# Kernel optimization log

Measured on AMD Instinct MI355X. Metric: run time of the kernel, lower is better.

Reference implementation:

```python
import jax, jax.numpy as jnp
import numpy as np

VERTS = [5023, 1256, 314, 79, 20]
SPIRAL_LEN = 9
T_FRAMES = 32
LATENT = 64


def _spiral_conv(x, idx, W, b):
    # x: [B, N, C]; idx: [N, L]; gather spiral neighborhoods then linear
    B = x.shape[0]
    g = x[:, idx.reshape(-1), :].reshape(B, idx.shape[0], -1)  # [B, N, L*C]
    return g @ W.T + b


def _pool(x, rows, cols, vals, n_out):
    # sparse matmul: out[b, rows] += x[b, cols] * vals  (index_select + scatter_add)
    gathered = x[:, cols, :] * vals[None, :, None]
    return jnp.zeros((x.shape[0], n_out, x.shape[2]), x.dtype).at[:, rows, :].add(gathered)


def _lstm_dir(x, Wih, Whh, bih, bhh, reverse):
    # x: [T, B, D]; PyTorch gate order i, f, g, o
    Bz, H = x.shape[1], Whh.shape[1]
    bias = bih + bhh
    def step(carry, xt):
        h, c = carry
        g = xt @ Wih.T + h @ Whh.T + bias
        i, f, gg, o = jnp.split(g, 4, axis=-1)
        c = jax.nn.sigmoid(f) * c + jax.nn.sigmoid(i) * jnp.tanh(gg)
        h = jax.nn.sigmoid(o) * jnp.tanh(c)
        return (h, c), h
    init = (jnp.zeros((Bz, H), x.dtype), jnp.zeros((Bz, H), x.dtype))
    _, hs = jax.lax.scan(step, init, x, reverse=reverse)
    return hs


def _forward(audio_hidden, vertices, actor,
             sp_idx0, sp_idx1, sp_idx2, sp_idx3,
             d0_rows, d0_cols, d0_vals, d1_rows, d1_cols, d1_vals,
             d2_rows, d2_cols, d2_vals, d3_rows, d3_cols, d3_vals,
             u0_rows, u0_cols, u0_vals, u1_rows, u1_cols, u1_vals,
             u2_rows, u2_cols, u2_vals, u3_rows, u3_cols, u3_vals,
             enc_W0, enc_b0, enc_W1, enc_b1, enc_W2, enc_b2, enc_W3, enc_b3,
             enc_lin_W, enc_lin_b, dec_lin_W, dec_lin_b,
             dec_W0, dec_b0, dec_W1, dec_b1, dec_W2, dec_b2, dec_W3, dec_b3,
             dec_W4, dec_b4, aud_W, aud_b,
             l0_Wih, l0_Whh, l0_bih, l0_bhh, l12_Wih, l12_Whh, l12_bih, l12_bhh):
    ah = audio_hidden
    if ah.shape[1] % 2 != 0:
        ah = ah[:, :ah.shape[1] - 1]
    tv = vertices.shape[1]
    if ah.shape[1] > 2 * tv:
        ah = ah[:, :2 * tv]
    elif ah.shape[1] < 2 * tv:
        tv = ah.shape[1] // 2
    hs = ah.reshape(1, ah.shape[1] // 2, ah.shape[2] * 2)[:, :tv]  # [1, T, 1536]
    audio_emb = hs @ aud_W.T + aud_b                                # [1, T, LATENT]
    # --- mesh encoder on actor template: (spiral conv -> ELU -> down pool) x4 -> Linear ---
    sp = (sp_idx0, sp_idx1, sp_idx2, sp_idx3)
    down = ((d0_rows, d0_cols, d0_vals), (d1_rows, d1_cols, d1_vals),
            (d2_rows, d2_cols, d2_vals), (d3_rows, d3_cols, d3_vals))
    encp = ((enc_W0, enc_b0), (enc_W1, enc_b1), (enc_W2, enc_b2), (enc_W3, enc_b3))
    x = actor
    for i in range(4):
        x = jax.nn.elu(_spiral_conv(x, sp[i], *encp[i]))
        x = _pool(x, *down[i], VERTS[i + 1])
    z = x.reshape(x.shape[0], -1) @ enc_lin_W.T + enc_lin_b        # [1, LATENT]
    actor_emb = jnp.broadcast_to(z[:, None, :], audio_emb.shape)
    # --- 3-layer bidirectional LSTM ---
    h = jnp.concatenate([audio_emb, actor_emb], axis=-1).transpose(1, 0, 2)  # [T, 1, 2*LATENT]
    for layer in range(3):
        if layer == 0:
            Wih, Whh, bih, bhh = l0_Wih, l0_Whh, l0_bih, l0_bhh
        else:
            Wih, Whh, bih, bhh = l12_Wih[layer - 1], l12_Whh[layer - 1], l12_bih[layer - 1], l12_bhh[layer - 1]
        f = _lstm_dir(h, Wih[0], Whh[0], bih[0], bhh[0], False)
        r = _lstm_dir(h, Wih[1], Whh[1], bih[1], bhh[1], True)
        h = jnp.concatenate([f, r], axis=-1)
    latent = h.transpose(1, 0, 2)[0]                               # [T, LATENT]
    # --- mesh decoder, batched over all frames (replaces the python per-frame loop) ---
    up = ((u0_rows, u0_cols, u0_vals), (u1_rows, u1_cols, u1_vals),
          (u2_rows, u2_cols, u2_vals), (u3_rows, u3_cols, u3_vals))
    decp = ((dec_W0, dec_b0), (dec_W1, dec_b1), (dec_W2, dec_b2), (dec_W3, dec_b3))
    y = latent @ dec_lin_W.T + dec_lin_b                           # [T, 20*256]
    y = y.reshape(y.shape[0], VERTS[4], -1)                        # [T, 20, 256]
    for i in range(4):
        j = 3 - i
        y = _pool(y, *up[j], VERTS[j])
        y = jax.nn.elu(_spiral_conv(y, sp[j], *decp[i]))
    y = _spiral_conv(y, sp[0], dec_W4, dec_b4)                     # [T, 5023, 3]
    return y + actor                                               # broadcast residual, == vstacked preds


def setup_inputs() -> dict:
    key = jax.random.key(0)
    ks = iter(jax.random.split(key, 96))
    def nrm(shape, s=0.05):
        return jax.random.normal(next(ks), shape, jnp.float32) * s
    def rint(shape, hi):
        return jax.random.randint(next(ks), shape, 0, hi)
    inp = {}
    inp['audio_hidden'] = nrm((1, 2 * T_FRAMES, 768), 1.0)
    inp['vertices'] = nrm((1, T_FRAMES, VERTS[0], 3), 1.0)
    inp['actor'] = nrm((1, VERTS[0], 3), 1.0)
    for i in range(4):
        inp['sp_idx%d' % i] = rint((VERTS[i], SPIRAL_LEN), VERTS[i])
    for i in range(4):
        nnz = 3 * VERTS[i + 1]
        inp['d%d_rows' % i] = rint((nnz,), VERTS[i + 1])
        inp['d%d_cols' % i] = rint((nnz,), VERTS[i])
        inp['d%d_vals' % i] = jax.random.uniform(next(ks), (nnz,), jnp.float32)
    for i in range(4):
        nnz = 3 * VERTS[i]
        inp['u%d_rows' % i] = rint((nnz,), VERTS[i])
        inp['u%d_cols' % i] = rint((nnz,), VERTS[i + 1])
        inp['u%d_vals' % i] = jax.random.uniform(next(ks), (nnz,), jnp.float32)
    OC = [32, 64, 128, 256]
    ic = 3
    for i in range(4):
        inp['enc_W%d' % i] = nrm((OC[i], ic * SPIRAL_LEN))
        inp['enc_b%d' % i] = nrm((OC[i],))
        ic = OC[i]
    inp['enc_lin_W'] = nrm((LATENT, VERTS[4] * OC[3]))
    inp['enc_lin_b'] = nrm((LATENT,))
    inp['dec_lin_W'] = nrm((VERTS[4] * OC[3], LATENT))
    inp['dec_lin_b'] = nrm((VERTS[4] * OC[3],))
    dic = [256, 256, 128, 64]
    doc = [256, 128, 64, 32]
    for i in range(4):
        inp['dec_W%d' % i] = nrm((doc[i], dic[i] * SPIRAL_LEN))
        inp['dec_b%d' % i] = nrm((doc[i],))
    inp['dec_W4'] = nrm((3, OC[0] * SPIRAL_LEN))
    inp['dec_b4'] = nrm((3,))
    inp['aud_W'] = nrm((LATENT, 1536))
    inp['aud_b'] = nrm((LATENT,))
    H = LATENT // 2
    inp['l0_Wih'] = nrm((2, 4 * H, 2 * LATENT))
    inp['l0_Whh'] = nrm((2, 4 * H, H))
    inp['l0_bih'] = nrm((2, 4 * H))
    inp['l0_bhh'] = nrm((2, 4 * H))
    inp['l12_Wih'] = nrm((2, 2, 4 * H, 2 * H))
    inp['l12_Whh'] = nrm((2, 2, 4 * H, H))
    inp['l12_bih'] = nrm((2, 2, 4 * H))
    inp['l12_bhh'] = nrm((2, 2, 4 * H))
    return inp


def reference(audio_hidden, vertices, actor,
              sp_idx0, sp_idx1, sp_idx2, sp_idx3,
              d0_rows, d0_cols, d0_vals, d1_rows, d1_cols, d1_vals,
              d2_rows, d2_cols, d2_vals, d3_rows, d3_cols, d3_vals,
              u0_rows, u0_cols, u0_vals, u1_rows, u1_cols, u1_vals,
              u2_rows, u2_cols, u2_vals, u3_rows, u3_cols, u3_vals,
              enc_W0, enc_b0, enc_W1, enc_b1, enc_W2, enc_b2, enc_W3, enc_b3,
              enc_lin_W, enc_lin_b, dec_lin_W, dec_lin_b,
              dec_W0, dec_b0, dec_W1, dec_b1, dec_W2, dec_b2, dec_W3, dec_b3,
              dec_W4, dec_b4, aud_W, aud_b,
              l0_Wih, l0_Whh, l0_bih, l0_bhh, l12_Wih, l12_Whh, l12_bih, l12_bhh):
    return _forward(audio_hidden, vertices, actor,
                    sp_idx0, sp_idx1, sp_idx2, sp_idx3,
                    d0_rows, d0_cols, d0_vals, d1_rows, d1_cols, d1_vals,
                    d2_rows, d2_cols, d2_vals, d3_rows, d3_cols, d3_vals,
                    u0_rows, u0_cols, u0_vals, u1_rows, u1_cols, u1_vals,
                    u2_rows, u2_cols, u2_vals, u3_rows, u3_cols, u3_vals,
                    enc_W0, enc_b0, enc_W1, enc_b1, enc_W2, enc_b2, enc_W3, enc_b3,
                    enc_lin_W, enc_lin_b, dec_lin_W, dec_lin_b,
                    dec_W0, dec_b0, dec_W1, dec_b1, dec_W2, dec_b2, dec_W3, dec_b3,
                    dec_W4, dec_b4, aud_W, aud_b,
                    l0_Wih, l0_Whh, l0_bih, l0_bhh, l12_Wih, l12_Whh, l12_bih, l12_bhh)
```

## Files before the change

kernel.cpp:

```cpp
#include <hip/hip_runtime.h>
#include <cstdint>
#include <cstddef>


typedef unsigned short u16;
typedef __attribute__((ext_vector_type(8))) short short8;
typedef __attribute__((ext_vector_type(4))) float float4v;
#define CDIV(a,b) (((a)+(b)-1)/(b))
#define POOL_CAP 64

__device__ __forceinline__ float bf(u16 u){ return __uint_as_float(((unsigned)u)<<16); }
__device__ __forceinline__ u16 fb(float x){
  unsigned u = __float_as_uint(x);
  unsigned r = u + 0x7fffu + ((u>>16)&1u);
  return (u16)(r>>16);
}
__device__ __forceinline__ float lo16(unsigned u){ return __uint_as_float(u<<16); }
__device__ __forceinline__ float hi16(unsigned u){ return __uint_as_float(u & 0xffff0000u); }

struct WCast { const float* src[7]; int cum[8]; };
struct Lists {
  const int* rows[8];
  int nnz[8];
  int curoff[8];
  int lstoff[8];
};

__global__ void __launch_bounds__(256) setup_k(
    Lists L, int totN, int NF, int* __restrict__ curBase, int* __restrict__ lstBase,
    WCast C, int totW, int NC, u16* __restrict__ Wbf,
    const float* __restrict__ audio, const float* __restrict__ audW,
    const float* __restrict__ audB, float* __restrict__ h0,
    const float* __restrict__ actor, const int* __restrict__ sp0,
    const float* __restrict__ encW0, const float* __restrict__ encB0,
    u16* __restrict__ outA){
  int blk = blockIdx.x;
  int tid = threadIdx.x;
  if (blk < NF){
    int i = blk*256 + tid;
    if (i < totN){
      int off = i, k = 0;
      while (off >= L.nnz[k]){ off -= L.nnz[k]; k++; }
      int r = L.rows[k][off];
      int p = atomicAdd(curBase + L.curoff[k] + r, 1);
      if (p < POOL_CAP) lstBase[L.lstoff[k] + r*POOL_CAP + p] = off;
    }
    return;
  }
  blk -= NF;
  if (blk < NC){
    int i = blk*256 + tid;
    if (i < totW){
      int k = 0;
      while (i >= C.cum[k+1]) k++;
      Wbf[i] = fb(C.src[k][i - C.cum[k]]);
    }
    return;
  }
  blk -= NC;
  if (blk < 32){
    int t = blk;
    int f = tid >> 2, sl = tid & 3;
    const float4* x4 = (const float4*)(audio + t*1536);
    const float4* w4 = (const float4*)(audW + f*1536);
    float acc = 0.f;
    for (int k=sl; k<384; k+=4){
      float4 xv = x4[k], wv = w4[k];
      acc += xv.x*wv.x + xv.y*wv.y + xv.z*wv.z + xv.w*wv.w;
    }
    acc += __shfl_down(acc, 2, 64);
    acc += __shfl_down(acc, 1, 64);
    if (sl == 0) h0[t*128 + f] = acc + audB[f];
    return;
  }
  blk -= 32;
  int i = blk*256 + tid;
  if (i >= 5023*32) return;
  int o = i % 32; int v = i / 32;
  const float* wrow = encW0 + (size_t)o*27;
  const int* vix = sp0 + v*9;
  float acc = encB0[o];
  for (int s=0;s<9;s++){
    const float* xr = actor + (size_t)vix[s]*3;
    acc += xr[0]*wrow[s*3] + xr[1]*wrow[s*3+1] + xr[2]*wrow[s*3+2];
  }
  if (acc < 0.f) acc = expm1f(acc);
  outA[i] = fb(acc);
}

template<int IC, int BN, int BM>
__global__ void __launch_bounds__(256) conv_mfma(
    const u16* __restrict__ x, const int* __restrict__ idx,
    const u16* __restrict__ Wb, const float* __restrict__ bias,
    u16* __restrict__ out, int V, int OC, int M){
  constexpr int K = 9*IC;
  constexpr int KC = K/32;
  constexpr int NT = BN/16;
  constexpr int MT = BM/64;
  constexpr int LOG2 = (IC==32?5: IC==64?6: IC==128?7:8);
  constexpr int AST = 40;
  __shared__ u16 Asm[2][BM*AST];
  __shared__ u16 Bsm[2][BN*AST];
  __shared__ int rowB[BM], rowV[BM];
  __shared__ int sidx[BM*9];
  int t = threadIdx.x;
  int m0 = blockIdx.x*BM;
  int o0 = blockIdx.y*BN;
  if (t < BM){
    int mg = m0 + t;
    if (mg < M){ int b = mg / V; rowB[t] = b; rowV[t] = mg - b*V; }
    else rowB[t] = -1;
  }
  __syncthreads();
  for (int i=t; i<BM*9; i+=256){
    int r = i/9, s = i - r*9;
    sidx[i] = (rowB[r] >= 0) ? idx[rowV[r]*9 + s] : 0;
  }
  int lane = t & 63, wave = t >> 6;
  int quad = lane >> 4, col = lane & 15;
  float4v acc[MT][NT];
  #pragma unroll
  for (int mi=0;mi<MT;mi++)
    #pragma unroll
    for (int nt=0;nt<NT;nt++) acc[mi][nt] = (float4v)0.f;

  uint4 aval[MT]; uint4 bval;
  auto fetch = [&](int kc){
    int s  = (kc*32) >> LOG2;
    int c0 = (kc*32) & (IC-1);
    #pragma unroll
    for (int rpt=0; rpt<MT; ++rpt){
      int seg = t + 256*rpt;
      int arow = seg >> 2, aq = seg & 3;
      int b = rowB[arow];
      uint4 v = {0u,0u,0u,0u};
      if (b >= 0){
        int ix = sidx[arow*9 + s];
        v = *(const uint4*)(x + ((size_t)b*V + ix)*IC + c0 + aq*8);
      }
      aval[rpt] = v;
    }
    if (t < BN*4){
      int br = t >> 2, bq = t & 3;
      bval = *(const uint4*)(Wb + (size_t)(o0+br)*K + kc*32 + bq*8);
    }
  };

  __syncthreads();
  fetch(0);

  for (int kc = 0; kc < KC; ++kc){
    int buf = kc & 1;
    #pragma unroll
    for (int rpt=0; rpt<MT; ++rpt){
      int seg = t + 256*rpt;
      int arow = seg >> 2, aq = seg & 3;
      *(uint4*)&Asm[buf][arow*AST + aq*8] = aval[rpt];
    }
    if (t < BN*4){
      int br = t >> 2, bq = t & 3;
      *(uint4*)&Bsm[buf][br*AST + bq*8] = bval;
    }
    __syncthreads();
    if (kc+1 < KC) fetch(kc+1);
    short8 a[MT];
    #pragma unroll
    for (int mi=0;mi<MT;mi++)
      a[mi] = *(const short8*)&Asm[buf][(wave*MT*16 + mi*16 + col)*AST + quad*8];
    #pragma unroll
    for (int nt=0; nt<NT; ++nt){
      short8 bfr = *(const short8*)&Bsm[buf][(nt*16 + col)*AST + quad*8];
      #pragma unroll
      for (int mi=0;mi<MT;mi++)
        acc[mi][nt] = __builtin_amdgcn_mfma_f32_16x16x32_bf16(a[mi], bfr, acc[mi][nt], 0, 0, 0);
    }
  }
  #pragma unroll
  for (int mi=0;mi<MT;mi++){
    #pragma unroll
    for (int nt=0; nt<NT; ++nt){
      int o = o0 + nt*16 + col;
      float bv = bias[o];
      #pragma unroll
      for (int r=0;r<4;r++){
        int mg = m0 + wave*MT*16 + mi*16 + quad*4 + r;
        if (mg < M){
          float val = acc[mi][nt][r] + bv;
          if (val < 0.f) val = expm1f(val);
          out[(size_t)mg*OC + o] = fb(val);
        }
      }
    }
  }
}

__global__ void pool_g8_k(const u16* __restrict__ x, const int* __restrict__ cols,
                          const float* __restrict__ vals, const int* __restrict__ cur,
                          const int* __restrict__ lst, u16* __restrict__ out,
                          int B, int Vin, int Vout, int C){
  int C8 = C >> 3;
  int total = B*Vout*C8;
  int i = blockIdx.x*blockDim.x + threadIdx.x;
  if (i >= total) return;
  int c8 = i % C8; int tt = i / C8; int r = tt % Vout; int b = tt / Vout;
  int deg = cur[r]; if (deg > POOL_CAP) deg = POOL_CAP;
  const int* le = lst + r*POOL_CAP;
  float a0=0.f,a1=0.f,a2=0.f,a3=0.f,a4=0.f,a5=0.f,a6=0.f,a7=0.f;
  for (int k=0;k<deg;k++){
    int e = le[k];
    float v = vals[e];
    uint4 xv = *(const uint4*)(x + ((size_t)b*Vin + (size_t)cols[e])*C + c8*8);
    a0 += v*lo16(xv.x); a1 += v*hi16(xv.x);
    a2 += v*lo16(xv.y); a3 += v*hi16(xv.y);
    a4 += v*lo16(xv.z); a5 += v*hi16(xv.z);
    a6 += v*lo16(xv.w); a7 += v*hi16(xv.w);
  }
  uint4 o;
  o.x = ((unsigned)fb(a0)) | (((unsigned)fb(a1))<<16);
  o.y = ((unsigned)fb(a2)) | (((unsigned)fb(a3))<<16);
  o.z = ((unsigned)fb(a4)) | (((unsigned)fb(a5))<<16);
  o.w = ((unsigned)fb(a6)) | (((unsigned)fb(a7))<<16);
  *(uint4*)(out + ((size_t)b*Vout + (size_t)r)*C + c8*8) = o;
}

__global__ void __launch_bounds__(256) enc_lin_k(
    const u16* __restrict__ x, const float* __restrict__ W,
    const float* __restrict__ b, float* __restrict__ h0){
  int f = blockIdx.x;
  int t = threadIdx.x;
  const ushort4* x4 = (const ushort4*)x;
  const float4* w4 = (const float4*)(W + (size_t)f*5120);
  float acc = 0.f;
  for (int k=t; k<1280; k+=256){
    ushort4 xv = x4[k]; float4 wv = w4[k];
    acc += bf(xv.x)*wv.x + bf(xv.y)*wv.y + bf(xv.z)*wv.z + bf(xv.w)*wv.w;
  }
  #pragma unroll
  for (int off=32; off; off>>=1) acc += __shfl_down(acc, off, 64);
  __shared__ float red[4];
  if ((t & 63) == 0) red[t>>6] = acc;
  __syncthreads();
  if (t < 32){
    float zf = b[f] + red[0] + red[1] + red[2] + red[3];
    h0[t*128 + 64 + f] = zf;
  }
}

__device__ __forceinline__ float sigm(float x){ return 1.f/(1.f+__expf(-x)); }
__device__ __forceinline__ float tanhfast(float x){ return 1.f - 2.f/(__expf(2.f*x)+1.f); }

__global__ void __launch_bounds__(256) lstm3_k(
    const float* __restrict__ h0,
    const float* __restrict__ l0_Wih, const float* __restrict__ l0_Whh,
    const float* __restrict__ l0_bih, const float* __restrict__ l0_bhh,
    const float* __restrict__ l12_Wih, const float* __restrict__ l12_Whh,
    const float* __restrict__ l12_bih, const float* __restrict__ l12_bhh,
    float* __restrict__ latent){
  __shared__ __align__(16) u16 xb[32*136];
  __shared__ __align__(16) float xp[2*32*128];
  __shared__ __align__(16) u16 obuf[32*64];
  __shared__ __align__(16) float hsh32[2][32];
  __shared__ float bias_l[256];
  int t = threadIdx.x;
  int lane = t & 63, wave = t >> 6;
  int quad = lane >> 4, col = lane & 15;

  for (int i=t;i<32*128;i+=256){ int tt=i>>7, k=i&127; xb[tt*136+k]=fb(h0[i]); }

  for (int layer=0; layer<3; layer++){
    int IN = (layer==0)?128:64;
    const float *Wih,*Whh,*bih,*bhh;
    if (layer==0){ Wih=l0_Wih; Whh=l0_Whh; bih=l0_bih; bhh=l0_bhh; }
    else {
      int mb=(layer-1)*2;
      Wih=l12_Wih + (size_t)mb*128*64; Whh=l12_Whh + (size_t)mb*128*32;
      bih=l12_bih + mb*128; bhh=l12_bhh + mb*128;
    }
    bias_l[t] = bih[(t>>7)*128 + (t&127)] + bhh[(t>>7)*128 + (t&127)];
    __syncthreads();

    {
      int dirA = wave >> 1, o0 = (wave & 1)*64;
      const float* WA = Wih + (size_t)dirA*128*IN;
      float4v acc[2][4];
      #pragma unroll
      for (int mi=0;mi<2;mi++)
        #pragma unroll
        for (int nt=0;nt<4;nt++) acc[mi][nt] = (float4v)0.f;
      for (int kc=0; kc<IN/32; ++kc){
        short8 bfrag[4];
        #pragma unroll
        for (int nt=0;nt<4;nt++){
          const float* src = WA + (size_t)(o0+nt*16+col)*IN + kc*32 + quad*8;
          float4 w0 = *(const float4*)src;
          float4 w1 = *(const float4*)(src+4);
          alignas(16) u16 tmp[8] = {fb(w0.x),fb(w0.y),fb(w0.z),fb(w0.w),
                                    fb(w1.x),fb(w1.y),fb(w1.z),fb(w1.w)};
          bfrag[nt] = *(const short8*)tmp;
        }
        short8 afrag[2];
        #pragma unroll
        for (int mi=0;mi<2;mi++)
          afrag[mi] = *(const short8*)&xb[(mi*16+col)*136 + kc*32 + quad*8];
        #pragma unroll
        for (int nt=0;nt<4;nt++)
          #pragma unroll
          for (int mi=0;mi<2;mi++)
            acc[mi][nt] = __builtin_amdgcn_mfma_f32_16x16x32_bf16(afrag[mi], bfrag[nt], acc[mi][nt], 0, 0, 0);
      }
      #pragma unroll
      for (int mi=0;mi<2;mi++)
        #pragma unroll
        for (int nt=0;nt<4;nt++){
          int j = o0 + nt*16 + col;
          float bv = bias_l[dirA*128 + j];
          #pragma unroll
          for (int r=0;r<4;r++){
            int tt = mi*16 + quad*4 + r;
            xp[dirA*4096 + tt*128 + j] = acc[mi][nt][r] + bv;
          }
        }
    }
    __syncthreads();

    if (wave < 2){
      int dir = wave; bool rev = (dir == 1);
      int unit = lane & 31, gh = lane >> 5;
      int jA = gh*32 + unit;
      int jB = (gh+2)*32 + unit;
      const float* WD = Whh + (size_t)dir*128*32;
      float wA[32], wB[32];
      #pragma unroll
      for (int k=0;k<32;k++){ wA[k]=WD[(size_t)jA*32+k]; wB[k]=WD[(size_t)jB*32+k]; }
      float* hsd = &hsh32[dir][0];
      if (gh==0) hsd[unit] = 0.f;
      float creg = 0.f;
      const float* xpd = xp + dir*4096;
      float gAc = xpd[(rev?31:0)*128 + jA];
      float gBc = xpd[(rev?31:0)*128 + jB];
      #pragma unroll 1
      for (int s=0;s<32;s++){
        int tx = rev ? (31-s) : s;
        int sn = (s+1 < 32) ? s+1 : 31;
        int txn = rev ? (31-sn) : sn;
        float gA2 = xpd[txn*128 + jA];
        float gB2 = xpd[txn*128 + jB];
        const float4* h4 = (const float4*)hsd;
        float a0=0.f,a1=0.f,a2=0.f,a3=0.f,b0=0.f,b1=0.f,b2=0.f,b3=0.f;
        #pragma unroll
        for (int k=0;k<8;k++){
          float4 hv = h4[k];
          a0=fmaf(hv.x,wA[4*k+0],a0); b0=fmaf(hv.x,wB[4*k+0],b0);
          a1=fmaf(hv.y,wA[4*k+1],a1); b1=fmaf(hv.y,wB[4*k+1],b1);
          a2=fmaf(hv.z,wA[4*k+2],a2); b2=fmaf(hv.z,wB[4*k+2],b2);
          a3=fmaf(hv.w,wA[4*k+3],a3); b3=fmaf(hv.w,wB[4*k+3],b3);
        }
        float gA = gAc + ((a0+a1)+(a2+a3));
        float gB = gBc + ((b0+b1)+(b2+b3));
        float actA = sigm(gA);
        float tB = sigm(gh ? gB : 2.f*gB);
        float actB = gh ? tB : (2.f*tB - 1.f);
        float pA = __shfl_xor(actA, 32, 64);
        float pB = __shfl_xor(actB, 32, 64);
        float gi = gh ? pA : actA;
        float gf = gh ? actA : pA;
        float gg = gh ? pB : actB;
        float go = gh ? actB : pB;
        float cn = fmaf(gf, creg, gi*gg);
        float hn = go * tanhfast(cn);
        creg = cn;
        if (gh==0){
          hsd[unit] = hn;
          obuf[tx*64 + dir*32 + unit] = fb(hn);
        }
        gAc = gA2; gBc = gB2;
      }
    }
    __syncthreads();
    if (layer < 2){
      for (int i=t;i<32*64;i+=256){ int tt=i>>6, k=i&63; xb[tt*136+k]=obuf[i]; }
      __syncthreads();
    }
  }
  for (int i=t;i<32*64;i+=256) latent[i] = bf(obuf[i]);
}

__global__ void dec_lin_k(const float* __restrict__ latent, const float* __restrict__ W,
                          const float* __restrict__ b, u16* __restrict__ y){
  int i = blockIdx.x*blockDim.x + threadIdx.x;
  if (i >= 32*5120) return;
  int r = i % 5120, t = i / 5120;
  const float4* x4 = (const float4*)(latent + t*64);
  const float4* w4 = (const float4*)(W + (size_t)r*64);
  float acc = b[r];
  #pragma unroll
  for (int k=0;k<16;k++){
    float4 xv=x4[k]; float4 wv=w4[k];
    acc += xv.x*wv.x+xv.y*wv.y+xv.z*wv.z+xv.w*wv.w;
  }
  y[i] = fb(acc);
}

__global__ void final_k(const u16* __restrict__ x, const int* __restrict__ idx,
                        const float* __restrict__ W, const float* __restrict__ bias,
                        const float* __restrict__ actor, float* __restrict__ out){
  __shared__ float Wsm[3*288];
  __shared__ float bsm[3];
  int t = threadIdx.x;
  for (int i=t;i<864;i+=256) Wsm[i]=W[i];
  if (t<3) bsm[t]=bias[t];
  __syncthreads();
  int g = blockIdx.x*256 + t;
  if (g >= 32*5023) return;
  int v = g % 5023, b = g / 5023;
  const u16* xb = x + (size_t)b*5023*32;
  const int* vix = idx + v*9;
  float a0=bsm[0], a1=bsm[1], a2=bsm[2];
  for (int s=0;s<9;s++){
    const ushort4* xr = (const ushort4*)(xb + (size_t)vix[s]*32);
    #pragma unroll
    for (int k=0;k<8;k++){
      ushort4 xv = xr[k];
      float x0=bf(xv.x), x1=bf(xv.y), x2=bf(xv.z), x3=bf(xv.w);
      int kk = s*32 + k*4;
      a0 += x0*Wsm[kk] + x1*Wsm[kk+1] + x2*Wsm[kk+2] + x3*Wsm[kk+3];
      a1 += x0*Wsm[288+kk] + x1*Wsm[288+kk+1] + x2*Wsm[288+kk+2] + x3*Wsm[288+kk+3];
      a2 += x0*Wsm[576+kk] + x1*Wsm[576+kk+1] + x2*Wsm[576+kk+2] + x3*Wsm[576+kk+3];
    }
  }
  out[(size_t)g*3+0] = a0 + actor[v*3+0];
  out[(size_t)g*3+1] = a1 + actor[v*3+1];
  out[(size_t)g*3+2] = a2 + actor[v*3+2];
}

extern "C" void kernel_launch(void* const* d_in, const int* in_sizes, int n_in,
                              void* d_out, int out_size, void* d_ws, size_t ws_size,
                              hipStream_t stream){
  (void)in_sizes; (void)n_in; (void)out_size; (void)ws_size;

  const float* audio = (const float*)d_in[0];
  const float* actor = (const float*)d_in[2];
  const int* sp[4]   = {(const int*)d_in[3],(const int*)d_in[4],(const int*)d_in[5],(const int*)d_in[6]};
  const int* drows[4]; const int* dcols[4]; const float* dvals[4];
  for (int i=0;i<4;i++){ drows[i]=(const int*)d_in[7+3*i]; dcols[i]=(const int*)d_in[8+3*i]; dvals[i]=(const float*)d_in[9+3*i]; }
  const int* urows[4]; const int* ucols[4]; const float* uvals[4];
  for (int i=0;i<4;i++){ urows[i]=(const int*)d_in[19+3*i]; ucols[i]=(const int*)d_in[20+3*i]; uvals[i]=(const float*)d_in[21+3*i]; }
  const float* encW[4]={(const float*)d_in[31],(const float*)d_in[33],(const float*)d_in[35],(const float*)d_in[37]};
  const float* encB[4]={(const float*)d_in[32],(const float*)d_in[34],(const float*)d_in[36],(const float*)d_in[38]};
  const float* enc_lin_W=(const float*)d_in[39]; const float* enc_lin_b=(const float*)d_in[40];
  const float* dec_lin_W=(const float*)d_in[41]; const float* dec_lin_b=(const float*)d_in[42];
  const float* decW[5]={(const float*)d_in[43],(const float*)d_in[45],(const float*)d_in[47],(const float*)d_in[49],(const float*)d_in[51]};
  const float* decB[5]={(const float*)d_in[44],(const float*)d_in[46],(const float*)d_in[48],(const float*)d_in[50],(const float*)d_in[52]};
  const float* audW=(const float*)d_in[53]; const float* audB=(const float*)d_in[54];
  const float* l0_Wih=(const float*)d_in[55]; const float* l0_Whh=(const float*)d_in[56];
  const float* l0_bih=(const float*)d_in[57]; const float* l0_bhh=(const float*)d_in[58];
  const float* l12_Wih=(const float*)d_in[59]; const float* l12_Whh=(const float*)d_in[60];
  const float* l12_bih=(const float*)d_in[61]; const float* l12_bhh=(const float*)d_in[62];
  float* out = (float*)d_out;

  char* base = (char*)d_ws;
  u16* A  = (u16*)base;
  u16* Bb = (u16*)(base + 10287104);
  int* curBase = (int*)(base + 30891520);
  int* lstBase = (int*)(base + 30924928);
  u16* Wbf = (u16*)(base + 33060224);
  float* sm = (float*)(base + 35788160);
  float* h0     = sm;
  float* latent = sm + 4096;

  const int wsz[7] = {64*288, 128*576, 256*1152, 256*2304, 128*2304, 64*1152, 32*576};
  WCast WC; int wcum = 0;
  const float* wsrc[7] = {encW[1],encW[2],encW[3],decW[0],decW[1],decW[2],decW[3]};
  int wo[7];
  for (int k=0;k<7;k++){ WC.src[k]=wsrc[k]; WC.cum[k]=wcum; wo[k]=wcum; wcum+=wsz[k]; }
  WC.cum[7]=wcum;

  const int pVout[8] = {1256,314,79,20,5023,1256,314,79};
  const int pNnz[8]  = {3768,942,237,60,15069,3768,942,237};
  Lists L; int curoff=0, lstoff=0, totnnz=0;
  const int* prow[8] = {drows[0],drows[1],drows[2],drows[3],urows[0],urows[1],urows[2],urows[3]};
  int curo[8], lsto[8];
  for (int k=0;k<8;k++){
    L.rows[k]=prow[k]; L.nnz[k]=pNnz[k];
    L.curoff[k]=curoff; L.lstoff[k]=lstoff;
    curo[k]=curoff; lsto[k]=lstoff;
    curoff += pVout[k]; lstoff += pVout[k]*POOL_CAP; totnnz += pNnz[k];
  }
  hipMemsetAsync(curBase, 0, (size_t)curoff*4, stream);

  int NF = CDIV(totnnz,256), NC = CDIV(wcum,256), NC3 = CDIV(5023*32,256);
  setup_k<<<NF+NC+32+NC3,256,0,stream>>>(L, totnnz, NF, curBase, lstBase,
                                         WC, wcum, NC, Wbf,
                                         audio, audW, audB, h0,
                                         actor, sp[0], encW[0], encB[0], A);

  pool_g8_k<<<CDIV(1256*4,256),256,0,stream>>>(A, dcols[0], dvals[0], curBase+curo[0], lstBase+lsto[0], Bb, 1, 5023, 1256, 32);
  conv_mfma<32,64,64><<<dim3(CDIV(1256,64),1),256,0,stream>>>(Bb, sp[1], Wbf+wo[0], encB[1], A, 1256, 64, 1256);
  pool_g8_k<<<CDIV(314*8,256),256,0,stream>>>(A, dcols[1], dvals[1], curBase+curo[1], lstBase+lsto[1], Bb, 1, 1256, 314, 64);
  conv_mfma<64,64,64><<<dim3(CDIV(314,64),2),256,0,stream>>>(Bb, sp[2], Wbf+wo[1], encB[2], A, 314, 128, 314);
  pool_g8_k<<<CDIV(79*16,256),256,0,stream>>>(A, dcols[2], dvals[2], curBase+curo[2], lstBase+lsto[2], Bb, 1, 314, 79, 128);
  conv_mfma<128,64,64><<<dim3(CDIV(79,64),4),256,0,stream>>>(Bb, sp[3], Wbf+wo[2], encB[3], A, 79, 256, 79);
  pool_g8_k<<<CDIV(20*32,256),256,0,stream>>>(A, dcols[3], dvals[3], curBase+curo[3], lstBase+lsto[3], Bb, 1, 79, 20, 256);

  enc_lin_k<<<64,256,0,stream>>>(Bb, enc_lin_W, enc_lin_b, h0);

  lstm3_k<<<1,256,0,stream>>>(h0, l0_Wih, l0_Whh, l0_bih, l0_bhh,
                              l12_Wih, l12_Whh, l12_bih, l12_bhh, latent);

  dec_lin_k<<<CDIV(32*5120,256),256,0,stream>>>(latent, dec_lin_W, dec_lin_b, A);

  pool_g8_k<<<CDIV(32*79*32,256),256,0,stream>>>(A, ucols[3], uvals[3], curBase+curo[7], lstBase+lsto[7], Bb, 32, 20, 79, 256);
  conv_mfma<256,64,64><<<dim3(CDIV(2528,64),4),256,0,stream>>>(Bb, sp[3], Wbf+wo[3], decB[0], A, 79, 256, 2528);

  pool_g8_k<<<CDIV(32*314*32,256),256,0,stream>>>(A, ucols[2], uvals[2], curBase+curo[6], lstBase+lsto[6], Bb, 32, 79, 314, 256);
  conv_mfma<256,64,64><<<dim3(CDIV(10048,64),2),256,0,stream>>>(Bb, sp[2], Wbf+wo[4], decB[1], A, 314, 128, 10048);

  pool_g8_k<<<CDIV(32*1256*16,256),256,0,stream>>>(A, ucols[1], uvals[1], curBase+curo[5], lstBase+lsto[5], Bb, 32, 314, 1256, 128);
  conv_mfma<128,64,128><<<dim3(CDIV(40192,128),1),256,0,stream>>>(Bb, sp[1], Wbf+wo[5], decB[2], A, 1256, 64, 40192);

  pool_g8_k<<<CDIV(32*5023*8,256),256,0,stream>>>(A, ucols[0], uvals[0], curBase+curo[4], lstBase+lsto[4], Bb, 32, 1256, 5023, 64);
  conv_mfma<64,32,128><<<dim3(CDIV(160736,128),1),256,0,stream>>>(Bb, sp[0], Wbf+wo[6], decB[3], A, 5023, 32, 160736);

  final_k<<<CDIV(32*5023,256),256,0,stream>>>(A, sp[0], decW[4], decB[4], actor, out);
}
```

Baseline: 569.2 us.

## Fuse encoder and decoder stages into persistent megakernels with grid barriers

Replaces the chain of separate pool, conv, linear and final launches with two persistent kernels, one for the encoder (64 blocks) and one for the decoder (256 blocks). Each stage loops over its tiles with a grid-stride loop, and stages are separated by atomic-counter grid barriers whose counters are reset in the setup kernel. The aim is to remove per-launch overhead and tail gaps between many small kernels. In exchange the decoder's large conv stages now run on only 256 blocks with a fixed static shared-memory footprint, which may cut parallelism and occupancy. The spin barriers also assume every block is co-resident on the GPU.

```diff
diff --git a/kernel.cpp b/kernel.cpp
--- a/kernel.cpp
+++ b/kernel.cpp
@@ -17,6 +17,18 @@
 }
 __device__ __forceinline__ float lo16(unsigned u){ return __uint_as_float(u<<16); }
 __device__ __forceinline__ float hi16(unsigned u){ return __uint_as_float(u & 0xffff0000u); }
+
+__device__ __forceinline__ void gsync(int* cnt, int nblk){
+  __syncthreads();
+  if (threadIdx.x == 0){
+    __threadfence();
+    atomicAdd(cnt, 1);
+    while (atomicAdd(cnt, 0) < nblk)
+      __builtin_amdgcn_s_sleep(8);
+    __threadfence();
+  }
+  __syncthreads();
+}
 
 struct WCast { const float* src[7]; int cum[8]; };
 struct Lists {
@@ -33,9 +45,10 @@
     const float* __restrict__ audB, float* __restrict__ h0,
     const float* __restrict__ actor, const int* __restrict__ sp0,
     const float* __restrict__ encW0, const float* __restrict__ encB0,
-    u16* __restrict__ outA){
+    u16* __restrict__ outA, int* __restrict__ bar){
   int blk = blockIdx.x;
   int tid = threadIdx.x;
+  if (blk == 0 && tid < 32) bar[tid] = 0;
   if (blk < NF){
     int i = blk*256 + tid;
     if (i < totN){
@@ -88,8 +101,37 @@
   outA[i] = fb(acc);
 }
 
+struct PoolP { const int* cols; const float* vals; const int* cur; const int* lst;
+               int B, Vin, Vout, C; };
+
+__device__ void pool_dev(const u16* __restrict__ x, PoolP p, u16* __restrict__ out){
+  int C8 = p.C >> 3;
+  int total = p.B*p.Vout*C8;
+  for (int i = blockIdx.x*256 + threadIdx.x; i < total; i += gridDim.x*256){
+    int c8 = i % C8; int tt = i / C8; int r = tt % p.Vout; int b = tt / p.Vout;
+    int deg = p.cur[r]; if (deg > POOL_CAP) deg = POOL_CAP;
+    const int* le = p.lst + r*POOL_CAP;
+    float a0=0.f,a1=0.f,a2=0.f,a3=0.f,a4=0.f,a5=0.f,a6=0.f,a7=0.f;
+    for (int k=0;k<deg;k++){
+      int e = le[k];
+      float v = p.vals[e];
+      uint4 xv = *(const uint4*)(x + ((size_t)b*p.Vin + (size_t)p.cols[e])*p.C + c8*8);
+      a0 += v*lo16(xv.x); a1 += v*hi16(xv.x);
+      a2 += v*lo16(xv.y); a3 += v*hi16(xv.y);
+      a4 += v*lo16(xv.z); a5 += v*hi16(xv.z);
+      a6 += v*lo16(xv.w); a7 += v*hi16(xv.w);
+    }
+    uint4 o;
+    o.x = ((unsigned)fb(a0)) | (((unsigned)fb(a1))<<16);
+    o.y = ((unsigned)fb(a2)) | (((unsigned)fb(a3))<<16);
+    o.z = ((unsigned)fb(a4)) | (((unsigned)fb(a5))<<16);
+    o.w = ((unsigned)fb(a6)) | (((unsigned)fb(a7))<<16);
+    *(uint4*)(out + ((size_t)b*p.Vout + (size_t)r)*p.C + c8*8) = o;
+  }
+}
+
 template<int IC, int BN, int BM>
-__global__ void __launch_bounds__(256) conv_mfma(
+__device__ void conv_dev(char* smem,
     const u16* __restrict__ x, const int* __restrict__ idx,
     const u16* __restrict__ Wb, const float* __restrict__ bias,
     u16* __restrict__ out, int V, int OC, int M){
@@ -99,151 +141,243 @@
   constexpr int MT = BM/64;
   constexpr int LOG2 = (IC==32?5: IC==64?6: IC==128?7:8);
   constexpr int AST = 40;
-  __shared__ u16 Asm[2][BM*AST];
-  __shared__ u16 Bsm[2][BN*AST];
-  __shared__ int rowB[BM], rowV[BM];
-  __shared__ int sidx[BM*9];
+  u16* Asm0 = (u16*)smem;
+  u16* Bsm0 = Asm0 + 2*BM*AST;
+  int* rowB = (int*)(Bsm0 + 2*BN*AST);
+  int* rowV = rowB + BM;
+  int* sidx = rowV + BM;
   int t = threadIdx.x;
-  int m0 = blockIdx.x*BM;
-  int o0 = blockIdx.y*BN;
-  if (t < BM){
-    int mg = m0 + t;
-    if (mg < M){ int b = mg / V; rowB[t] = b; rowV[t] = mg - b*V; }
-    else rowB[t] = -1;
-  }
-  __syncthreads();
-  for (int i=t; i<BM*9; i+=256){
-    int r = i/9, s = i - r*9;
-    sidx[i] = (rowB[r] >= 0) ? idx[rowV[r]*9 + s] : 0;
-  }
   int lane = t & 63, wave = t >> 6;
   int quad = lane >> 4, col = lane & 15;
-  float4v acc[MT][NT];
-  #pragma unroll
-  for (int mi=0;mi<MT;mi++)
-    #pragma unroll
-    for (int nt=0;nt<NT;nt++) acc[mi][nt] = (float4v)0.f;
-
-  uint4 aval[MT]; uint4 bval;
-  auto fetch = [&](int kc){
-    int s  = (kc*32) >> LOG2;
-    int c0 = (kc*32) & (IC-1);
-    #pragma unroll
-    for (int rpt=0; rpt<MT; ++rpt){
-      int seg = t + 256*rpt;
-      int arow = seg >> 2, aq = seg & 3;
-      int b = rowB[arow];
-      uint4 v = {0u,0u,0u,0u};
-      if (b >= 0){
-        int ix = sidx[arow*9 + s];
-        v = *(const uint4*)(x + ((size_t)b*V + ix)*IC + c0 + aq*8);
-      }
-      aval[rpt] = v;
-    }
-    if (t < BN*4){
-      int br = t >> 2, bq = t & 3;
-      bval = *(const uint4*)(Wb + (size_t)(o0+br)*K + kc*32 + bq*8);
-    }
-  };
-
-  __syncthreads();
-  fetch(0);
-
-  for (int kc = 0; kc < KC; ++kc){
-    int buf = kc & 1;
-    #pragma unroll
-    for (int rpt=0; rpt<MT; ++rpt){
-      int seg = t + 256*rpt;
-      int arow = seg >> 2, aq = seg & 3;
-      *(uint4*)&Asm[buf][arow*AST + aq*8] = aval[rpt];
-    }
-    if (t < BN*4){
-      int br = t >> 2, bq = t & 3;
-      *(uint4*)&Bsm[buf][br*AST + bq*8] = bval;
+  int ntx = (M + BM - 1)/BM, nty = OC/BN;
+  int ntiles = ntx*nty;
+
+  for (int tile = blockIdx.x; tile < ntiles; tile += gridDim.x){
+    int m0 = (tile % ntx)*BM;
+    int o0 = (tile / ntx)*BN;
+    if (t < BM){
+      int mg = m0 + t;
+      if (mg < M){ int b = mg / V; rowB[t] = b; rowV[t] = mg - b*V; }
+      else rowB[t] = -1;
     }
     __syncthreads();
-    if (kc+1 < KC) fetch(kc+1);
-    short8 a[MT];
+    for (int i=t; i<BM*9; i+=256){
+      int r = i/9, s = i - r*9;
+      sidx[i] = (rowB[r] >= 0) ? idx[rowV[r]*9 + s] : 0;
+    }
+    float4v acc[MT][NT];
     #pragma unroll
     for (int mi=0;mi<MT;mi++)
-      a[mi] = *(const short8*)&Asm[buf][(wave*MT*16 + mi*16 + col)*AST + quad*8];
+      #pragma unroll
+      for (int nt=0;nt<NT;nt++) acc[mi][nt] = (float4v)0.f;
+
+    uint4 aval[MT]; uint4 bval;
+    auto fetch = [&](int kc){
+      int s  = (kc*32) >> LOG2;
+      int c0 = (kc*32) & (IC-1);
+      #pragma unroll
+      for (int rpt=0; rpt<MT; ++rpt){
+        int seg = t + 256*rpt;
+        int arow = seg >> 2, aq = seg & 3;
+        int b = rowB[arow];
+        uint4 v = {0u,0u,0u,0u};
+        if (b >= 0){
+          int ix = sidx[arow*9 + s];
+          v = *(const uint4*)(x + ((size_t)b*V + ix)*IC + c0 + aq*8);
+        }
+        aval[rpt] = v;
+      }
+      if (t < BN*4){
+        int br = t >> 2, bq = t & 3;
+        bval = *(const uint4*)(Wb + (size_t)(o0+br)*K + kc*32 + bq*8);
+      }
+    };
+
+    __syncthreads();
+    fetch(0);
+
+    for (int kc = 0; kc < KC; ++kc){
+      int buf = kc & 1;
+      #pragma unroll
+      for (int rpt=0; rpt<MT; ++rpt){
+        int seg = t + 256*rpt;
+        int arow = seg >> 2, aq = seg & 3;
+        *(uint4*)&Asm0[buf*BM*AST + arow*AST + aq*8] = aval[rpt];
+      }
+      if (t < BN*4){
+        int br = t >> 2, bq = t & 3;
+        *(uint4*)&Bsm0[buf*BN*AST + br*AST + bq*8] = bval;
+      }
+      __syncthreads();
+      if (kc+1 < KC) fetch(kc+1);
+      short8 a[MT];
+      #pragma unroll
+      for (int mi=0;mi<MT;mi++)
+        a[mi] = *(const short8*)&Asm0[buf*BM*AST + (wave*MT*16 + mi*16 + col)*AST + quad*8];
+      #pragma unroll
+      for (int nt=0; nt<NT; ++nt){
+        short8 bfr = *(const short8*)&Bsm0[buf*BN*AST + (nt*16 + col)*AST + quad*8];
+        #pragma unroll
+        for (int mi=0;mi<MT;mi++)
+          acc[mi][nt] = __builtin_amdgcn_mfma_f32_16x16x32_bf16(a[mi], bfr, acc[mi][nt], 0, 0, 0);
+      }
+    }
     #pragma unroll
-    for (int nt=0; nt<NT; ++nt){
-      short8 bfr = *(const short8*)&Bsm[buf][(nt*16 + col)*AST + quad*8];
-      #pragma unroll
-      for (int mi=0;mi<MT;mi++)
-        acc[mi][nt] = __builtin_amdgcn_mfma_f32_16x16x32_bf16(a[mi], bfr, acc[mi][nt], 0, 0, 0);
-    }
-  }
-  #pragma unroll
-  for (int mi=0;mi<MT;mi++){
+    for (int mi=0;mi<MT;mi++){
+      #pragma unroll
+      for (int nt=0; nt<NT; ++nt){
+        int o = o0 + nt*16 + col;
+        float bv = bias[o];
+        #pragma unroll
+        for (int r=0;r<4;r++){
+          int mg = m0 + wave*MT*16 + mi*16 + quad*4 + r;
+          if (mg < M){
+            float val = acc[mi][nt][r] + bv;
+            if (val < 0.f) val = expm1f(val);
+            out[(size_t)mg*OC + o] = fb(val);
+          }
+        }
+      }
+    }
+  }
+}
+
+__device__ void enc_lin_dev(char* smem, const u16* __restrict__ x,
+                            const float* __restrict__ W, const float* __restrict__ b,
+                            float* __restrict__ h0){
+  float* red = (float*)smem;
+  int t = threadIdx.x;
+  for (int f = blockIdx.x; f < 64; f += gridDim.x){
+    const ushort4* x4 = (const ushort4*)x;
+    const float4* w4 = (const float4*)(W + (size_t)f*5120);
+    float acc = 0.f;
+    for (int k=t; k<1280; k+=256){
+      ushort4 xv = x4[k]; float4 wv = w4[k];
+      acc += bf(xv.x)*wv.x + bf(xv.y)*wv.y + bf(xv.z)*wv.z + bf(xv.w)*wv.w;
+    }
     #pragma unroll
-    for (int nt=0; nt<NT; ++nt){
-      int o = o0 + nt*16 + col;
-      float bv = bias[o];
-      #pragma unroll
-      for (int r=0;r<4;r++){
-        int mg = m0 + wave*MT*16 + mi*16 + quad*4 + r;
-        if (mg < M){
-          float val = acc[mi][nt][r] + bv;
-          if (val < 0.f) val = expm1f(val);
-          out[(size_t)mg*OC + o] = fb(val);
-        }
-      }
-    }
-  }
-}
-
-__global__ void pool_g8_k(const u16* __restrict__ x, const int* __restrict__ cols,
-                          const float* __restrict__ vals, const int* __restrict__ cur,
-                          const int* __restrict__ lst, u16* __restrict__ out,
-                          int B, int Vin, int Vout, int C){
-  int C8 = C >> 3;
-  int total = B*Vout*C8;
-  int i = blockIdx.x*blockDim.x + threadIdx.x;
-  if (i >= total) return;
-  int c8 = i % C8; int tt = i / C8; int r = tt % Vout; int b = tt / Vout;
-  int deg = cur[r]; if (deg > POOL_CAP) deg = POOL_CAP;
-  const int* le = lst + r*POOL_CAP;
-  float a0=0.f,a1=0.f,a2=0.f,a3=0.f,a4=0.f,a5=0.f,a6=0.f,a7=0.f;
-  for (int k=0;k<deg;k++){
-    int e = le[k];
-    float v = vals[e];
-    uint4 xv = *(const uint4*)(x + ((size_t)b*Vin + (size_t)cols[e])*C + c8*8);
-    a0 += v*lo16(xv.x); a1 += v*hi16(xv.x);
-    a2 += v*lo16(xv.y); a3 += v*hi16(xv.y);
-    a4 += v*lo16(xv.z); a5 += v*hi16(xv.z);
-    a6 += v*lo16(xv.w); a7 += v*hi16(xv.w);
-  }
-  uint4 o;
-  o.x = ((unsigned)fb(a0)) | (((unsigned)fb(a1))<<16);
-  o.y = ((unsigned)fb(a2)) | (((unsigned)fb(a3))<<16);
-  o.z = ((unsigned)fb(a4)) | (((unsigned)fb(a5))<<16);
-  o.w = ((unsigned)fb(a6)) | (((unsigned)fb(a7))<<16);
-  *(uint4*)(out + ((size_t)b*Vout + (size_t)r)*C + c8*8) = o;
-}
-
-__global__ void __launch_bounds__(256) enc_lin_k(
-    const u16* __restrict__ x, const float* __restrict__ W,
-    const float* __restrict__ b, float* __restrict__ h0){
-  int f = blockIdx.x;
+    for (int off=32; off; off>>=1) acc += __shfl_down(acc, off, 64);
+    if ((t & 63) == 0) red[t>>6] = acc;
+    __syncthreads();
+    if (t < 32){
+      float zf = b[f] + red[0] + red[1] + red[2] + red[3];
+      h0[t*128 + 64 + f] = zf;
+    }
+    __syncthreads();
+  }
+}
+
+__device__ void dec_lin_dev(const float* __restrict__ latent, const float* __restrict__ W,
+                            const float* __restrict__ b, u16* __restrict__ y){
+  for (int i = blockIdx.x*256 + threadIdx.x; i < 32*5120; i += gridDim.x*256){
+    int r = i % 5120, tt = i / 5120;
+    const float4* x4 = (const float4*)(latent + tt*64);
+    const float4* w4 = (const float4*)(W + (size_t)r*64);
+    float acc = b[r];
+    #pragma unroll
+    for (int k=0;k<16;k++){
+      float4 xv=x4[k]; float4 wv=w4[k];
+      acc += xv.x*wv.x+xv.y*wv.y+xv.z*wv.z+xv.w*wv.w;
+    }
+    y[i] = fb(acc);
+  }
+}
+
+__device__ void final_dev(char* smem, const u16* __restrict__ x, const int* __restrict__ idx,
+                          const float* __restrict__ W, const float* __restrict__ bias,
+                          const float* __restrict__ actor, float* __restrict__ out){
+  float* Wsm = (float*)smem;
+  float* bsm = Wsm + 864;
   int t = threadIdx.x;
-  const ushort4* x4 = (const ushort4*)x;
-  const float4* w4 = (const float4*)(W + (size_t)f*5120);
-  float acc = 0.f;
-  for (int k=t; k<1280; k+=256){
-    ushort4 xv = x4[k]; float4 wv = w4[k];
-    acc += bf(xv.x)*wv.x + bf(xv.y)*wv.y + bf(xv.z)*wv.z + bf(xv.w)*wv.w;
-  }
-  #pragma unroll
-  for (int off=32; off; off>>=1) acc += __shfl_down(acc, off, 64);
-  __shared__ float red[4];
-  if ((t & 63) == 0) red[t>>6] = acc;
+  for (int i=t;i<864;i+=256) Wsm[i]=W[i];
+  if (t<3) bsm[t]=bias[t];
   __syncthreads();
-  if (t < 32){
-    float zf = b[f] + red[0] + red[1] + red[2] + red[3];
-    h0[t*128 + 64 + f] = zf;
-  }
+  for (int g = blockIdx.x*256 + t; g < 32*5023; g += gridDim.x*256){
+    int v = g % 5023, b = g / 5023;
+    const u16* xb = x + (size_t)b*5023*32;
+    const int* vix = idx + v*9;
+    float a0=bsm[0], a1=bsm[1], a2=bsm[2];
+    for (int s=0;s<9;s++){
+      const ushort4* xr = (const ushort4*)(xb + (size_t)vix[s]*32);
+      #pragma unroll
+      for (int k=0;k<8;k++){
+        ushort4 xv = xr[k];
+        float x0=bf(xv.x), x1=bf(xv.y), x2=bf(xv.z), x3=bf(xv.w);
+        int kk = s*32 + k*4;
+        a0 += x0*Wsm[kk] + x1*Wsm[kk+1] + x2*Wsm[kk+2] + x3*Wsm[kk+3];
+        a1 += x0*Wsm[288+kk] + x1*Wsm[288+kk+1] + x2*Wsm[288+kk+2] + x3*Wsm[288+kk+3];
+        a2 += x0*Wsm[576+kk] + x1*Wsm[576+kk+1] + x2*Wsm[576+kk+2] + x3*Wsm[576+kk+3];
+      }
+    }
+    out[(size_t)g*3+0] = a0 + actor[v*3+0];
+    out[(size_t)g*3+1] = a1 + actor[v*3+1];
+    out[(size_t)g*3+2] = a2 + actor[v*3+2];
+  }
+}
+
+struct EncP {
+  u16 *A, *Bb;
+  PoolP p0, p1, p2, p3;
+  const int *sp1, *sp2, *sp3;
+  const u16 *w1, *w2, *w3;
+  const float *eb1, *eb2, *eb3;
+  const float *elW, *elb; float* h0;
+  int* bar;
+};
+
+__global__ void __launch_bounds__(256) enc_mega_k(EncP P){
+  __shared__ __align__(16) char smem[23552];
+  int nb = gridDim.x;
+  pool_dev(P.A, P.p0, P.Bb);
+  gsync(P.bar+0, nb);
+  conv_dev<32,64,64>(smem, P.Bb, P.sp1, P.w1, P.eb1, P.A, 1256, 64, 1256);
+  gsync(P.bar+1, nb);
+  pool_dev(P.A, P.p1, P.Bb);
+  gsync(P.bar+2, nb);
+  conv_dev<64,64,64>(smem, P.Bb, P.sp2, P.w2, P.eb2, P.A, 314, 128, 314);
+  gsync(P.bar+3, nb);
+  pool_dev(P.A, P.p2, P.Bb);
+  gsync(P.bar+4, nb);
+  conv_dev<128,64,64>(smem, P.Bb, P.sp3, P.w3, P.eb3, P.A, 79, 256, 79);
+  gsync(P.bar+5, nb);
+  pool_dev(P.A, P.p3, P.Bb);
+  gsync(P.bar+6, nb);
+  enc_lin_dev(smem, P.Bb, P.elW, P.elb, P.h0);
+}
+
+struct DecP {
+  const float* latent; const float* dlW; const float* dlb;
+  u16 *A, *Bb;
+  PoolP p3, p2, p1, p0;
+  const int *sp3, *sp2, *sp1, *sp0;
+  const u16 *w3, *w2, *w1, *w0;
+  const float *db0, *db1, *db2, *db3;
+  const float *fW, *fB; const float* actor; float* out;
+  int* bar;
+};
+
+__global__ void __launch_bounds__(256) dec_mega_k(DecP P){
+  __shared__ __align__(16) char smem[36608];
+  int nb = gridDim.x;
+  dec_lin_dev(P.latent, P.dlW, P.dlb, P.A);
+  gsync(P.bar+8, nb);
+  pool_dev(P.A, P.p3, P.Bb);
+  gsync(P.bar+9, nb);
+  conv_dev<256,64,64>(smem, P.Bb, P.sp3, P.w3, P.db0, P.A, 79, 256, 2528);
+  gsync(P.bar+10, nb);
+  pool_dev(P.A, P.p2, P.Bb);
+  gsync(P.bar+11, nb);
+  conv_dev<256,64,64>(smem, P.Bb, P.sp2, P.w2, P.db1, P.A, 314, 128, 10048);
+  gsync(P.bar+12, nb);
+  pool_dev(P.A, P.p1, P.Bb);
+  gsync(P.bar+13, nb);
+  conv_dev<128,64,128>(smem, P.Bb, P.sp1, P.w1, P.db2, P.A, 1256, 64, 40192);
+  gsync(P.bar+14, nb);
+  pool_dev(P.A, P.p0, P.Bb);
+  gsync(P.bar+15, nb);
+  conv_dev<64,32,128>(smem, P.Bb, P.sp0, P.w0, P.db3, P.A, 5023, 32, 160736);
+  gsync(P.bar+16, nb);
+  final_dev(smem, P.A, P.sp0, P.fW, P.fB, P.actor, P.out);
 }
 
 __device__ __forceinline__ float sigm(float x){ return 1.f/(1.f+__expf(-x)); }
@@ -385,54 +519,6 @@
   for (int i=t;i<32*64;i+=256) latent[i] = bf(obuf[i]);
 }
 
-__global__ void dec_lin_k(const float* __restrict__ latent, const float* __restrict__ W,
-                          const float* __restrict__ b, u16* __restrict__ y){
-  int i = blockIdx.x*blockDim.x + threadIdx.x;
-  if (i >= 32*5120) return;
-  int r = i % 5120, t = i / 5120;
-  const float4* x4 = (const float4*)(latent + t*64);
-  const float4* w4 = (const float4*)(W + (size_t)r*64);
-  float acc = b[r];
-  #pragma unroll
-  for (int k=0;k<16;k++){
-    float4 xv=x4[k]; float4 wv=w4[k];
-    acc += xv.x*wv.x+xv.y*wv.y+xv.z*wv.z+xv.w*wv.w;
-  }
-  y[i] = fb(acc);
-}
-
-__global__ void final_k(const u16* __restrict__ x, const int* __restrict__ idx,
-                        const float* __restrict__ W, const float* __restrict__ bias,
-                        const float* __restrict__ actor, float* __restrict__ out){
-  __shared__ float Wsm[3*288];
-  __shared__ float bsm[3];
-  int t = threadIdx.x;
-  for (int i=t;i<864;i+=256) Wsm[i]=W[i];
-  if (t<3) bsm[t]=bias[t];
-  __syncthreads();
-  int g = blockIdx.x*256 + t;
-  if (g >= 32*5023) return;
-  int v = g % 5023, b = g / 5023;
-  const u16* xb = x + (size_t)b*5023*32;
-  const int* vix = idx + v*9;
-  float a0=bsm[0], a1=bsm[1], a2=bsm[2];
-  for (int s=0;s<9;s++){
-    const ushort4* xr = (const ushort4*)(xb + (size_t)vix[s]*32);
-    #pragma unroll
-    for (int k=0;k<8;k++){
-      ushort4 xv = xr[k];
-      float x0=bf(xv.x), x1=bf(xv.y), x2=bf(xv.z), x3=bf(xv.w);
-      int kk = s*32 + k*4;
-      a0 += x0*Wsm[kk] + x1*Wsm[kk+1] + x2*Wsm[kk+2] + x3*Wsm[kk+3];
-      a1 += x0*Wsm[288+kk] + x1*Wsm[288+kk+1] + x2*Wsm[288+kk+2] + x3*Wsm[288+kk+3];
-      a2 += x0*Wsm[576+kk] + x1*Wsm[576+kk+1] + x2*Wsm[576+kk+2] + x3*Wsm[576+kk+3];
-    }
-  }
-  out[(size_t)g*3+0] = a0 + actor[v*3+0];
-  out[(size_t)g*3+1] = a1 + actor[v*3+1];
-  out[(size_t)g*3+2] = a2 + actor[v*3+2];
-}
-
 extern "C" void kernel_launch(void* const* d_in, const int* in_sizes, int n_in,
                               void* d_out, int out_size, void* d_ws, size_t ws_size,
                               hipStream_t stream){
@@ -467,6 +553,7 @@
   float* sm = (float*)(base + 35788160);
   float* h0     = sm;
   float* latent = sm + 4096;
+  int* barCnt = (int*)(base + 35812736);
 
   const int wsz[7] = {64*288, 128*576, 256*1152, 256*2304, 128*2304, 64*1152, 32*576};
   WCast WC; int wcum = 0;
@@ -492,34 +579,36 @@
   setup_k<<<NF+NC+32+NC3,256,0,stream>>>(L, totnnz, NF, curBase, lstBase,
                                          WC, wcum, NC, Wbf,
                                          audio, audW, audB, h0,
-                                         actor, sp[0], encW[0], encB[0], A);
-
-  pool_g8_k<<<CDIV(1256*4,256),256,0,stream>>>(A, dcols[0], dvals[0], curBase+curo[0], lstBase+lsto[0], Bb, 1, 5023, 1256, 32);
-  conv_mfma<32,64,64><<<dim3(CDIV(1256,64),1),256,0,stream>>>(Bb, sp[1], Wbf+wo[0], encB[1], A, 1256, 64, 1256);
-  pool_g8_k<<<CDIV(314*8,256),256,0,stream>>>(A, dcols[1], dvals[1], curBase+curo[1], lstBase+lsto[1], Bb, 1, 1256, 314, 64);
-  conv_mfma<64,64,64><<<dim3(CDIV(314,64),2),256,0,stream>>>(Bb, sp[2], Wbf+wo[1], encB[2], A, 314, 128, 314);
-  pool_g8_k<<<CDIV(79*16,256),256,0,stream>>>(A, dcols[2], dvals[2], curBase+curo[2], lstBase+lsto[2], Bb, 1, 314, 79, 128);
-  conv_mfma<128,64,64><<<dim3(CDIV(79,64),4),256,0,stream>>>(Bb, sp[3], Wbf+wo[2], encB[3], A, 79, 256, 79);
-  pool_g8_k<<<CDIV(20*32,256),256,0,stream>>>(A, dcols[3], dvals[3], curBase+curo[3], lstBase+lsto[3], Bb, 1, 79, 20, 256);
-
-  enc_lin_k<<<64,256,0,stream>>>(Bb, enc_lin_W, enc_lin_b, h0);
+                                         actor, sp[0], encW[0], encB[0],
+                                         A, barCnt);
+
+  EncP ep;
+  ep.A = A; ep.Bb = Bb;
+  ep.p0 = {dcols[0], dvals[0], curBase+curo[0], lstBase+lsto[0], 1, 5023, 1256, 32};
+  ep.p1 = {dcols[1], dvals[1], curBase+curo[1], lstBase+lsto[1], 1, 1256, 314, 64};
+  ep.p2 = {dcols[2], dvals[2], curBase+curo[2], lstBase+lsto[2], 1, 314, 79, 128};
+  ep.p3 = {dcols[3], dvals[3], curBase+curo[3], lstBase+lsto[3], 1, 79, 20, 256};
+  ep.sp1 = sp[1]; ep.sp2 = sp[2]; ep.sp3 = sp[3];
+  ep.w1 = Wbf+wo[0]; ep.w2 = Wbf+wo[1]; ep.w3 = Wbf+wo[2];
+  ep.eb1 = encB[1]; ep.eb2 = encB[2]; ep.eb3 = encB[3];
+  ep.elW = enc_lin_W; ep.elb = enc_lin_b; ep.h0 = h0;
+  ep.bar = barCnt;
+  enc_mega_k<<<64,256,0,stream>>>(ep);
 
   lstm3_k<<<1,256,0,stream>>>(h0, l0_Wih, l0_Whh, l0_bih, l0_bhh,
                               l12_Wih, l12_Whh, l12_bih, l12_bhh, latent);
 
-  dec_lin_k<<<CDIV(32*5120,256),256,0,stream>>>(latent, dec_lin_W, dec_lin_b, A);
-
-  pool_g8_k<<<CDIV(32*79*32,256),256,0,stream>>>(A, ucols[3], uvals[3], curBase+curo[7], lstBase+lsto[7], Bb, 32, 20, 79, 256);
-  conv_mfma<256,64,64><<<dim3(CDIV(2528,64),4),256,0,stream>>>(Bb, sp[3], Wbf+wo[3], decB[0], A, 79, 256, 2528);
-
-  pool_g8_k<<<CDIV(32*314*32,256),256,0,stream>>>(A, ucols[2], uvals[2], curBase+curo[6], lstBase+lsto[6], Bb, 32, 79, 314, 256);
-  conv_mfma<256,64,64><<<dim3(CDIV(10048,64),2),256,0,stream>>>(Bb, sp[2], Wbf+wo[4], decB[1], A, 314, 128, 10048);
-
-  pool_g8_k<<<CDIV(32*1256*16,256),256,0,stream>>>(A, ucols[1], uvals[1], curBase+curo[5], lstBase+lsto[5], Bb, 32, 314, 1256, 128);
-  conv_mfma<128,64,128><<<dim3(CDIV(40192,128),1),256,0,stream>>>(Bb, sp[1], Wbf+wo[5], decB[2], A, 1256, 64, 40192);
-
-  pool_g8_k<<<CDIV(32*5023*8,256),256,0,stream>>>(A, ucols[0], uvals[0], curBase+curo[4], lstBase+lsto[4], Bb, 32, 1256, 5023, 64);
-  conv_mfma<64,32,128><<<dim3(CDIV(160736,128),1),256,0,stream>>>(Bb, sp[0], Wbf+wo[6], decB[3], A, 5023, 32, 160736);
-
-  final_k<<<CDIV(32*5023,256),256,0,stream>>>(A, sp[0], decW[4], decB[4], actor, out);
-}
+  DecP dp;
+  dp.latent = latent; dp.dlW = dec_lin_W; dp.dlb = dec_lin_b;
+  dp.A = A; dp.Bb = Bb;
+  dp.p3 = {ucols[3], uvals[3], curBase+curo[7], lstBase+lsto[7], 32, 20, 79, 256};
+  dp.p2 = {ucols[2], uvals[2], curBase+curo[6], lstBase+lsto[6], 32, 79, 314, 256};
+  dp.p1 = {ucols[1], uvals[1], curBase+curo[5], lstBase+lsto[5], 32, 314, 1256, 128};
+  dp.p0 = {ucols[0], uvals[0], curBase+curo[4], lstBase+lsto[4], 32, 1256, 5023, 64};
+  dp.sp3 = sp[3]; dp.sp2 = sp[2]; dp.sp1 = sp[1]; dp.sp0 = sp[0];
+  dp.w3 = Wbf+wo[3]; dp.w2 = Wbf+wo[4]; dp.w1 = Wbf+wo[5]; dp.w0 = Wbf+wo[6];
+  dp.db0 = decB[0]; dp.db1 = decB[1]; dp.db2 = decB[2]; dp.db3 = decB[3];
+  dp.fW = decW[4]; dp.fB = decB[4]; dp.actor = actor; dp.out = out;
+  dp.bar = barCnt;
+  dec_mega_k<<<256,256,0,stream>>>(dp);
+}
```

Result: slower. 955.5 us (+67.9%).
